# Kernel optimization log

Hardware: AMD Instinct MI355X
Metric: run time of the kernel (lower is better)

Reference implementation:

```python
import jax, jax.numpy as jnp
import numpy as np

G, N, H = 64, 512, 64          # graphs, nodes/graph, hidden
NT = G * N                     # total nodes
DEG = 32
ET = NT * DEG                  # total edges
KP = int(np.ceil(0.7 * N))     # TopKPooling keep per graph (359)
NP2 = G * KP                   # nodes after pooling
F_IN, NC, NA = 128, 2, 6
seg = jax.ops.segment_sum


def graph_norm(h, batch, num_g, w, b, ms, eps=1e-5):
    cnt = seg(jnp.ones((h.shape[0], 1), h.dtype), batch, num_segments=num_g)
    mean = seg(h, batch, num_segments=num_g) / cnt
    hc = h - ms * mean[batch]
    var = seg(hc * hc, batch, num_segments=num_g) / cnt
    return w * hc / jnp.sqrt(var[batch] + eps) + b


def sage(h, src, tgt, valid, Ws, Wn, b, n_nodes):
    # PyG SAGEConv (mean aggr): out_i = x_i@Ws + mean_{j->i} x_j @ Wn + b
    msg = h[src] * valid[:, None]
    agg = seg(msg, tgt, num_segments=n_nodes)
    deg = seg(valid, tgt, num_segments=n_nodes)
    return h @ Ws + (agg / jnp.maximum(deg, 1.0)[:, None]) @ Wn + b


def setup_inputs() -> dict:
    key = jax.random.key(0)
    ks = jax.random.split(key, 20)
    offs = (jnp.arange(G) * N)[:, None]
    src = (jax.random.randint(ks[0], (G, N * DEG), 0, N) + offs).reshape(-1)
    tgt = (jax.random.randint(ks[1], (G, N * DEG), 0, N) + offs).reshape(-1)
    edge_index = jnp.stack([src, tgt])  # within-graph edges

    def lin(k, fi, fo):
        return jax.random.normal(k, (fi, fo), jnp.float32) / np.sqrt(fi)

    return {
        "x": jax.random.normal(ks[2], (NT, F_IN), jnp.float32),
        "edge_index": edge_index,
        "edge_attr": jax.random.uniform(ks[3], (ET,), jnp.float32),
        "coords": jax.random.normal(ks[4], (NT, 3), jnp.float32),
        "anatomical_class": jax.random.randint(ks[5], (NT,), 0, NA),
        "Bk_table": jax.random.normal(ks[6], (NA, H * H), jnp.float32) * 0.05,
        "pos_W": lin(ks[7], 3, H), "pos_b": jnp.zeros((H,), jnp.float32),
        "W1_self": lin(ks[8], F_IN, H), "W1_neigh": lin(ks[9], F_IN, H),
        "b1": jnp.zeros((H,), jnp.float32),
        "gn1_w": jnp.ones((H,), jnp.float32), "gn1_b": jnp.zeros((H,), jnp.float32),
        "gn1_ms": jnp.ones((H,), jnp.float32),
        "pool_p": jax.random.normal(ks[10], (H,), jnp.float32),
        "W2_self": lin(ks[11], H, H), "W2_neigh": lin(ks[12], H, H),
        "b2": jnp.zeros((H,), jnp.float32),
        "gn2_w": jnp.ones((H,), jnp.float32), "gn2_b": jnp.zeros((H,), jnp.float32),
        "gn2_ms": jnp.ones((H,), jnp.float32),
        "lin1_W": lin(ks[13], 3 * H, H), "lin1_b": jnp.zeros((H,), jnp.float32),
        "lin2_W": lin(ks[14], H, NC), "lin2_b": jnp.zeros((NC,), jnp.float32),
    }


def reference(x, edge_index, edge_attr, coords, anatomical_class, Bk_table,
              pos_W, pos_b, W1_self, W1_neigh, b1, gn1_w, gn1_b, gn1_ms,
              pool_p, W2_self, W2_neigh, b2, gn2_w, gn2_b, gn2_ms,
              lin1_W, lin1_b, lin2_W, lin2_b):
    row, col = edge_index[0], edge_index[1]
    batch = jnp.repeat(jnp.arange(G), N)
    # ---- stage 1: anatomical propagation kernel ----
    e = coords @ pos_W + pos_b                                 # [NT, H]
    Ae = seg(edge_attr[:, None] * e[col], row, num_segments=NT)  # SpMM adj @ e
    Bk = Bk_table[anatomical_class].reshape(NT, H, H)
    delta = jnp.einsum('nd,nhd->nh', Ae, Bk)                   # bmm(Ae, Bk^T)
    ones_e = jnp.ones((ET,), x.dtype)
    h = sage(x, row, col, ones_e, W1_self, W1_neigh, b1, NT)
    h = jax.nn.elu(graph_norm(h, batch, G, gn1_w, gn1_b, gn1_ms))
    h = h + delta
    h = jnp.einsum('nij,nj->ni', Bk + delta[:, :, None], h)    # propagate_message
    # ---- TopK pooling (equal-sized graphs) ----
    score = (h @ pool_p) / jnp.linalg.norm(pool_p)
    vals, idx = jax.lax.top_k(score.reshape(G, N), KP)
    perm = (idx + (jnp.arange(G) * N)[:, None]).reshape(-1)    # [NP2]
    h = h[perm] * jnp.tanh(vals).reshape(-1)[:, None]
    batch2 = jnp.repeat(jnp.arange(G), KP)
    node_map = jnp.full((NT,), -1, jnp.int32).at[perm].set(jnp.arange(NP2, dtype=jnp.int32))
    s2, t2 = node_map[row], node_map[col]
    valid = ((s2 >= 0) & (t2 >= 0)).astype(h.dtype)            # masked edge filter
    s2 = jnp.where(s2 >= 0, s2, 0)
    t2 = jnp.where(t2 >= 0, t2, 0)
    # ---- stage 2 ----
    e2 = coords[perm] @ pos_W + pos_b
    Bk2 = Bk_table[anatomical_class[perm]].reshape(NP2, H, H)
    Ae2 = seg(valid[:, None] * e2[t2], s2, num_segments=NP2)   # edge_attr = ones
    delta2 = jnp.einsum('nd,nhd->nh', Ae2, Bk2)
    h = h + delta2
    h = jnp.einsum('nij,nj->ni', Bk2 + delta2[:, :, None], h)
    h = sage(h, s2, t2, valid, W2_self, W2_neigh, b2, NP2)
    h = jax.nn.elu(graph_norm(h, batch2, G, gn2_w, gn2_b, gn2_ms))
    # ---- readout ----
    cnt = seg(jnp.ones((NP2, 1), h.dtype), batch2, num_segments=G)
    hsum = seg(h, batch2, num_segments=G)
    g = jnp.concatenate([hsum / cnt,
                         jax.ops.segment_max(h, batch2, num_segments=G),
                         hsum], axis=1)
    g = jax.nn.relu(g @ lin1_W + lin1_b)
    return jax.nn.log_softmax(g @ lin2_W + lin2_b, axis=1)
```

## Files before the change

kernel.cpp:

```cpp
#include <hip/hip_runtime.h>
#include <math.h>

#define G_    64
#define N_    512
#define NT_   32768
#define ET_   1048576
#define EPG_  16384
#define KP_   359
#define NP2_  22976
#define FIN_  128

__global__ __launch_bounds__(256)
void k_histprep(const int* __restrict__ row, const int* __restrict__ col,
                int* __restrict__ histR8, int* __restrict__ histC8,
                const float* __restrict__ Bk, const float* __restrict__ posW,
                const float* __restrict__ posb,
                float* __restrict__ BkT, float* __restrict__ PT) {
    int b = blockIdx.x, t = threadIdx.x;
    if (b < 512) {
        __shared__ int hr[N_], hc[N_];
        int g = b >> 3, s = b & 7;
        for (int i = t; i < N_; i += 256) { hr[i] = 0; hc[i] = 0; }
        __syncthreads();
        int ebase = g * EPG_ + s * 2048;
        for (int i = t; i < 2048; i += 256) {
            atomicAdd(&hr[row[ebase + i] & (N_ - 1)], 1);
            atomicAdd(&hc[col[ebase + i] & (N_ - 1)], 1);
        }
        __syncthreads();
        int sbase = b * N_;
        for (int i = t; i < N_; i += 256) {
            histR8[sbase + i] = hr[i];
            histC8[sbase + i] = hc[i];
        }
    } else if (b < 608) {
        int idx = (b - 512) * 256 + t;
        int c = idx >> 12, r = idx & 4095;
        int h = r >> 6, d = r & 63;
        BkT[c*4096 + d*64 + h] = Bk[c*4096 + h*64 + d];
    } else {
        int c = b - 608;
        int i = t >> 6, h = t & 63;
        const float* B = Bk + c*4096 + h*64;
        float acc = 0.f;
        for (int d = 0; d < 64; d++) {
            float vd = (i < 3) ? posW[i*64 + d] : posb[d];
            acc += B[d] * vd;
        }
        PT[c*256 + i*64 + h] = acc;
    }
}

__global__ __launch_bounds__(256)
void k_gemm_dual(const float* __restrict__ in, int K,
                 const float* __restrict__ Wa, const float* __restrict__ Wb,
                 const float* __restrict__ bias,
                 float* __restrict__ outA, float* __restrict__ outB) {
    __shared__ float inT[32 * FIN_];
    int row0 = blockIdx.x * 32;
    int t = threadIdx.x;
    for (int idx = t; idx < 32 * K; idx += 256) inT[idx] = in[row0 * K + idx];
    __syncthreads();
    int c = t & 63, rb = t >> 6;
    const float* ip = inT + (rb * 8) * K;
    float aA[8] = {0,0,0,0,0,0,0,0};
    float aB[8] = {0,0,0,0,0,0,0,0};
    for (int k = 0; k < K; k += 4) {
        float wa0 = Wa[(k+0)*64 + c], wa1 = Wa[(k+1)*64 + c];
        float wa2 = Wa[(k+2)*64 + c], wa3 = Wa[(k+3)*64 + c];
        float wb0 = Wb[(k+0)*64 + c], wb1 = Wb[(k+1)*64 + c];
        float wb2 = Wb[(k+2)*64 + c], wb3 = Wb[(k+3)*64 + c];
        #pragma unroll
        for (int r = 0; r < 8; r++) {
            float4 xv = *(const float4*)&ip[r*K + k];
            aA[r] += xv.x*wa0; aB[r] += xv.x*wb0;
            aA[r] += xv.y*wa1; aB[r] += xv.y*wb1;
            aA[r] += xv.z*wa2; aB[r] += xv.z*wb2;
            aA[r] += xv.w*wa3; aB[r] += xv.w*wb3;
        }
    }
    float bv = bias[c];
    #pragma unroll
    for (int r = 0; r < 8; r++) {
        int node = row0 + rb*8 + r;
        outA[node*64 + c] = aA[r];
        outB[node*64 + c] = aB[r] + bv;
    }
}

__global__ __launch_bounds__(1024)
void k_scatfuse(const int* __restrict__ row, const int* __restrict__ col,
                const float* __restrict__ ea,
                const int* __restrict__ histR8, const int* __restrict__ histC8,
                const float* __restrict__ coords, const float* __restrict__ y,
                const float* __restrict__ hself,
                int2* __restrict__ rowcsr, int* __restrict__ colcsr,
                int* __restrict__ rowptr, int* __restrict__ colptr,
                float* __restrict__ deg, int* __restrict__ nmap,
                float4* __restrict__ nsum, float* __restrict__ agg,
                float* __restrict__ statsP) {
    __shared__ int hr[N_], hc[N_];
    __shared__ int rst[128], rcn[128], cst[128], ccn[128];
    __shared__ float red[2048];
    int g = blockIdx.x >> 2, q = blockIdx.x & 3;
    int t = threadIdx.x;
    int lo = q * 128;
    int nbase = g * N_, ebase = g * EPG_;
    for (int i = t; i < N_; i += 1024) {
        int sr = 0, sc = 0;
        #pragma unroll
        for (int s = 0; s < 8; s++) {
            sr += histR8[(g*8 + s)*N_ + i];
            sc += histC8[(g*8 + s)*N_ + i];
        }
        hr[i] = sr; hc[i] = sc;
    }
    __syncthreads();
    int wave = t >> 6, lane = t & 63;
    if (wave < 2) {
        int* h = wave ? hc : hr;
        int base8 = lane * 8;
        int loc[8];
        int tot = 0;
        #pragma unroll
        for (int i = 0; i < 8; i++) { int v = h[base8 + i]; loc[i] = tot; tot += v; }
        int pref = tot;
        for (int off = 1; off < 64; off <<= 1) {
            int u = __shfl_up(pref, off);
            if (lane >= off) pref += u;
        }
        pref -= tot;
        #pragma unroll
        for (int i = 0; i < 8; i++) h[base8 + i] = pref + loc[i];
    }
    __syncthreads();
    if (t < 128) {
        int i = lo + t;
        int rs = hr[i];
        int re = (i < N_ - 1) ? hr[i + 1] : EPG_;
        int cs = hc[i];
        int ce = (i < N_ - 1) ? hc[i + 1] : EPG_;
        rst[t] = ebase + rs; rcn[t] = re - rs;
        cst[t] = ebase + cs; ccn[t] = ce - cs;
        rowptr[nbase + i] = ebase + rs;
        colptr[nbase + i] = ebase + cs;
        deg[nbase + i] = (float)(ce - cs);
        nmap[nbase + i] = -1;
    }
    if (blockIdx.x == 0 && t == 0) { rowptr[NT_] = ET_; colptr[NT_] = ET_; }
    __syncthreads();
    for (int i = t; i < EPG_; i += 1024) {
        int rg = row[ebase + i];
        int cg = col[ebase + i];
        int rl = (rg & (N_ - 1)) - lo;
        if ((unsigned)rl < 128u) {
            int pr = atomicAdd(&hr[lo + rl], 1);
            rowcsr[ebase + pr] = make_int2(cg, __float_as_int(ea[ebase + i]));
        }
        int cl = (cg & (N_ - 1)) - lo;
        if ((unsigned)cl < 128u) {
            int pc = atomicAdd(&hc[lo + cl], 1);
            colcsr[ebase + pc] = rg;
        }
    }
    __threadfence_block();
    __syncthreads();
    float s1 = 0.f, s2 = 0.f;
    #pragma unroll
    for (int r = 0; r < 8; r++) {
        int li   = wave * 8 + r;
        int node = nbase + lo + li;
        int rs = rst[li], rc = rcn[li];
        float sx = 0.f, sy = 0.f, sz = 0.f, sw = 0.f;
        for (int k = lane; k < rc; k += 64) {
            int2 ent = rowcsr[rs + k];
            int c = ent.x;
            float w = __int_as_float(ent.y);
            sx += w * coords[c*3+0];
            sy += w * coords[c*3+1];
            sz += w * coords[c*3+2];
            sw += w;
        }
        #pragma unroll
        for (int off = 32; off; off >>= 1) {
            sx += __shfl_xor(sx, off); sy += __shfl_xor(sy, off);
            sz += __shfl_xor(sz, off); sw += __shfl_xor(sw, off);
        }
        if (lane == 0) nsum[node] = make_float4(sx, sy, sz, sw);
        int cs = cst[li], cc = ccn[li];
        float acc = 0.f;
        #pragma unroll 8
        for (int k = 0; k < cc; k++) {
            int rr = colcsr[cs + k];
            acc += y[rr*64 + lane];
        }
        agg[node*64 + lane] = acc;
        float v = hself[node*64 + lane] + acc / fmaxf((float)cc, 1.f);
        s1 += v; s2 += v * v;
    }
    red[wave*64 + lane]        = s1;
    red[1024 + wave*64 + lane] = s2;
    __syncthreads();
    if (t < 64) {
        float a1 = 0.f, a2 = 0.f;
        #pragma unroll
        for (int wv = 0; wv < 16; wv++) {
            a1 += red[wv*64 + t];
            a2 += red[1024 + wv*64 + t];
        }
        statsP[blockIdx.x*128 + t]      = a1;
        statsP[blockIdx.x*128 + 64 + t] = a2;
    }
}

__global__ __launch_bounds__(256)
void k_gnstat(const float* __restrict__ hs, const float* __restrict__ agg,
              const float* __restrict__ deg, float* __restrict__ partial,
              int NPG, int CH, int npc) {
    __shared__ float r1[256], r2[256];
    int b = blockIdx.x;
    int g = b / CH, chunk = b % CH;
    int t = threadIdx.x, c = t & 63, grp = t >> 6;
    int n0 = chunk * npc;
    int nend = min(n0 + npc, NPG);
    float s1 = 0.f, s2 = 0.f;
    for (int n = n0 + grp; n < nend; n += 4) {
        int node = g * NPG + n;
        float v = hs[node*64 + c] + agg[node*64 + c] / fmaxf(deg[node], 1.f);
        s1 += v; s2 += v * v;
    }
    r1[t] = s1; r2[t] = s2;
    __syncthreads();
    if (grp == 0) {
        partial[b*128 + c]      = r1[c] + r1[64+c] + r1[128+c] + r1[192+c];
        partial[b*128 + 64 + c] = r2[c] + r2[64+c] + r2[128+c] + r2[192+c];
    }
}

__global__ __launch_bounds__(256)
void k_gnprop(const float* __restrict__ hself, const float* __restrict__ agg,
              const float* __restrict__ deg, const float* __restrict__ partial,
              const float* __restrict__ ms,
              const float* __restrict__ w, const float* __restrict__ b,
              const float4* __restrict__ nsum, const int* __restrict__ cls,
              const float* __restrict__ PT, const float* __restrict__ BkT,
              float* __restrict__ out) {
    __shared__ float hT[256];
    int t = threadIdx.x;
    int node = blockIdx.x * 4 + (t >> 6);
    int lane = t & 63;
    int g = (blockIdx.x * 4) >> 9;
    float s1 = 0.f, s2 = 0.f;
    #pragma unroll
    for (int i = 0; i < 4; i++) {
        s1 += partial[(g*4 + i)*128 + lane];
        s2 += partial[(g*4 + i)*128 + 64 + lane];
    }
    float m  = s1 / (float)N_, q = s2 / (float)N_, msv = ms[lane];
    float var = q - msv * m * m * (2.f - msv);
    float mval = msv * m;
    float istd = rsqrtf(var + 1e-5f);
    float4 s4 = nsum[node];
    int c = cls[node];
    const float* P = PT + c * 256;
    float d = s4.x*P[lane] + s4.y*P[64+lane] + s4.z*P[128+lane] + s4.w*P[192+lane];
    float v = hself[node*64 + lane] + agg[node*64 + lane] / fmaxf(deg[node], 1.f);
    v = w[lane] * (v - mval) * istd + b[lane];
    v = v > 0.f ? v : expm1f(v);
    v += d;
    hT[t] = v;
    __syncthreads();
    float ssum = v;
    #pragma unroll
    for (int off = 32; off; off >>= 1) ssum += __shfl_xor(ssum, off);
    const float* B  = BkT + c * 4096;
    const float* hv = hT + (t & ~63);
    float acc = 0.f;
    #pragma unroll 8
    for (int j = 0; j < 64; j++) acc += B[j*64 + lane] * hv[j];
    out[node*64 + lane] = acc + d * ssum;
}

__global__ __launch_bounds__(512)
void k_topk(const float* __restrict__ hp, const float* __restrict__ p,
            const int* __restrict__ cls, const int* __restrict__ ccsr,
            const int* __restrict__ row, const int* __restrict__ col,
            int* __restrict__ perm, float* __restrict__ tanhv,
            int* __restrict__ node_map, int* __restrict__ class2,
            int* __restrict__ ccsr2, float* __restrict__ deg2) {
    __shared__ float key[N_];
    __shared__ int   idxS[N_];
    __shared__ int   lmap[N_];
    __shared__ int   ideg[KP_];
    __shared__ float pS[64];
    __shared__ float nrm;
    int g = blockIdx.x, t = threadIdx.x;
    lmap[t] = -1;
    if (t < 64) pS[t] = p[t];
    for (int i = t; i < KP_; i += 512) ideg[i] = 0;
    __syncthreads();
    if (t == 0) {
        float s = 0.f;
        for (int i = 0; i < 64; i++) s += pS[i] * pS[i];
        nrm = sqrtf(s);
    }
    __syncthreads();
    {
        float acc = 0.f;
        const float* hv = hp + (size_t)(g*N_ + t) * 64;
        for (int cdx = 0; cdx < 64; cdx++) acc += hv[cdx] * pS[cdx];
        key[t]  = acc / nrm;
        idxS[t] = t;
    }
    __syncthreads();
    for (int k = 2; k <= N_; k <<= 1) {
        for (int j = k >> 1; j > 0; j >>= 1) {
            int i = t, ixj = i ^ j;
            if (ixj > i) {
                float ki = key[i], kj = key[ixj];
                int   ii = idxS[i], ij = idxS[ixj];
                bool before = (ki > kj) || (ki == kj && ii < ij);
                bool dir = ((i & k) == 0);
                if (dir ? !before : before) {
                    key[i] = kj; key[ixj] = ki;
                    idxS[i] = ij; idxS[ixj] = ii;
                }
            }
            __syncthreads();
        }
    }
    if (t < KP_) {
        int orig  = idxS[t];
        int gnode = g * N_ + orig;
        int pj    = g * KP_ + t;
        perm[pj]     = gnode;
        tanhv[pj]    = tanhf(key[t]);
        node_map[gnode] = pj;
        class2[pj]   = cls[gnode];
        lmap[orig]   = pj;
    }
    __syncthreads();
    int ebase = g * EPG_;
    for (int k = t; k < EPG_; k += 512) {
        int mm = lmap[ccsr[ebase + k] & (N_ - 1)];
        ccsr2[ebase + k] = (mm >= 0) ? mm : NP2_;
    }
    for (int k = t; k < EPG_; k += 512) {
        int mr = lmap[row[ebase + k] & (N_ - 1)];
        int mc = lmap[col[ebase + k] & (N_ - 1)];
        if (mr >= 0 && mc >= 0) atomicAdd(&ideg[mc - g * KP_], 1);
    }
    __syncthreads();
    for (int i = t; i < KP_; i += 512) deg2[g * KP_ + i] = (float)ideg[i];
}

__global__ __launch_bounds__(256)
void k_s2prop(const int* __restrict__ rowptr, const int2* __restrict__ rcsr,
              const int* __restrict__ perm, const int* __restrict__ nmap,
              const float* __restrict__ coords,
              const float* __restrict__ hp, const float* __restrict__ tanhv,
              const int* __restrict__ cls2,
              const float* __restrict__ PT, const float* __restrict__ BkT,
              float* __restrict__ out, float* __restrict__ y2zero) {
    __shared__ float hT[256];
    int t = threadIdx.x;
    int j = blockIdx.x * 4 + (t >> 6);
    int lane = t & 63;
    if (blockIdx.x == 0 && t < 64) y2zero[t] = 0.f;
    int orig = perm[j];
    int rs = rowptr[orig], re = rowptr[orig + 1];
    float sx = 0.f, sy = 0.f, sz = 0.f, sw = 0.f;
    for (int k = rs + lane; k < re; k += 64) {
        int c = rcsr[k].x;
        if (nmap[c] >= 0) {
            sx += coords[c*3+0]; sy += coords[c*3+1]; sz += coords[c*3+2];
            sw += 1.f;
        }
    }
    #pragma unroll
    for (int off = 32; off; off >>= 1) {
        sx += __shfl_xor(sx, off); sy += __shfl_xor(sy, off);
        sz += __shfl_xor(sz, off); sw += __shfl_xor(sw, off);
    }
    int c = cls2[j];
    const float* P = PT + c * 256;
    float d = sx*P[lane] + sy*P[64+lane] + sz*P[128+lane] + sw*P[192+lane];
    float v = hp[orig*64 + lane] * tanhv[j] + d;
    hT[t] = v;
    __syncthreads();
    float ssum = v;
    #pragma unroll
    for (int off = 32; off; off >>= 1) ssum += __shfl_xor(ssum, off);
    const float* B  = BkT + c * 4096;
    const float* hv = hT + (t & ~63);
    float acc = 0.f;
    #pragma unroll 8
    for (int jj = 0; jj < 64; jj++) acc += B[jj*64 + lane] * hv[jj];
    out[j*64 + lane] = acc + d * ssum;
}

__global__ __launch_bounds__(256)
void k_gagg2(const int* __restrict__ colptr, const int* __restrict__ ccsr2,
             const int* __restrict__ perm, const float* __restrict__ y2,
             float* __restrict__ agg2) {
    int j = blockIdx.x * 4 + (threadIdx.x >> 6);
    int lane = threadIdx.x & 63;
    int orig = perm[j];
    int start = colptr[orig], end = colptr[orig + 1];
    float acc = 0.f;
    #pragma unroll 8
    for (int k = start; k < end; k++) {
        int r = ccsr2[k];
        acc += y2[r*64 + lane];
    }
    agg2[j*64 + lane] = acc;
}

__global__ __launch_bounds__(256)
void k_gnrd(const float* __restrict__ hs, const float* __restrict__ agg,
            const float* __restrict__ deg2, const float* __restrict__ statsP,
            const float* __restrict__ ms,
            const float* __restrict__ w, const float* __restrict__ b,
            float* __restrict__ readP) {
    __shared__ float r1[256], r2[256];
    int blk = blockIdx.x;
    int g = blk / 6, chunk = blk % 6;
    int t = threadIdx.x, c = t & 63, grp = t >> 6;
    float s1 = 0.f, s2 = 0.f;
    #pragma unroll
    for (int i = 0; i < 6; i++) {
        s1 += statsP[(g*6 + i)*128 + c];
        s2 += statsP[(g*6 + i)*128 + 64 + c];
    }
    float mean = s1 / (float)KP_, q = s2 / (float)KP_, msv = ms[c];
    float var = q - msv * mean * mean * (2.f - msv);
    float mv = msv * mean;
    float is = rsqrtf(var + 1e-5f);
    float wv = w[c], bv = b[c];
    int n0 = chunk * 60, nend = min(n0 + 60, KP_);
    float s = 0.f, m = -1e30f;
    for (int n = n0 + grp; n < nend; n += 4) {
        int node = g * KP_ + n;
        float v = hs[node*64 + c] + agg[node*64 + c] / fmaxf(deg2[node], 1.f);
        v = wv * (v - mv) * is + bv;
        v = v > 0.f ? v : expm1f(v);
        s += v; m = fmaxf(m, v);
    }
    r1[t] = s; r2[t] = m;
    __syncthreads();
    if (grp == 0) {
        readP[blk*128 + c]      = r1[c] + r1[64+c] + r1[128+c] + r1[192+c];
        readP[blk*128 + 64 + c] = fmaxf(fmaxf(r2[c], r2[64+c]), fmaxf(r2[128+c], r2[192+c]));
    }
}

__global__ void k_rfin(const float* __restrict__ part, int CH,
                       const float* __restrict__ l1W, const float* __restrict__ l1b,
                       const float* __restrict__ l2W, const float* __restrict__ l2b,
                       float* __restrict__ out) {
    __shared__ float gv[192], rS[64];
    int g = blockIdx.x, t = threadIdx.x;
    float s = 0.f, m = -1e30f;
    for (int i = 0; i < CH; i++) {
        s += part[(g*CH + i)*128 + t];
        m = fmaxf(m, part[(g*CH + i)*128 + 64 + t]);
    }
    gv[t] = s / (float)KP_;
    gv[64 + t] = m;
    gv[128 + t] = s;
    __syncthreads();
    float acc = l1b[t];
    for (int k = 0; k < 192; k++) acc += gv[k] * l1W[k*64 + t];
    rS[t] = fmaxf(acc, 0.f);
    __syncthreads();
    if (t == 0) {
        float l0 = l2b[0], l1v = l2b[1];
        for (int hh = 0; hh < 64; hh++) { l0 += rS[hh]*l2W[hh*2+0]; l1v += rS[hh]*l2W[hh*2+1]; }
        float mx  = fmaxf(l0, l1v);
        float lse = mx + logf(expf(l0 - mx) + expf(l1v - mx));
        out[g*2 + 0] = l0  - lse;
        out[g*2 + 1] = l1v - lse;
    }
}

extern "C" void kernel_launch(void* const* d_in, const int* in_sizes, int n_in,
                              void* d_out, int out_size, void* d_ws, size_t ws_size,
                              hipStream_t stream) {
    const float* x      = (const float*)d_in[0];
    const int*   eidx   = (const int*)  d_in[1];
    const float* eattr  = (const float*)d_in[2];
    const float* coords = (const float*)d_in[3];
    const int*   acls   = (const int*)  d_in[4];
    const float* BkTab  = (const float*)d_in[5];
    const float* posW   = (const float*)d_in[6];
    const float* posb   = (const float*)d_in[7];
    const float* W1s    = (const float*)d_in[8];
    const float* W1n    = (const float*)d_in[9];
    const float* b1     = (const float*)d_in[10];
    const float* gn1w   = (const float*)d_in[11];
    const float* gn1b   = (const float*)d_in[12];
    const float* gn1ms  = (const float*)d_in[13];
    const float* poolp  = (const float*)d_in[14];
    const float* W2s    = (const float*)d_in[15];
    const float* W2n    = (const float*)d_in[16];
    const float* b2     = (const float*)d_in[17];
    const float* gn2w   = (const float*)d_in[18];
    const float* gn2b   = (const float*)d_in[19];
    const float* gn2ms  = (const float*)d_in[20];
    const float* l1W    = (const float*)d_in[21];
    const float* l1b    = (const float*)d_in[22];
    const float* l2W    = (const float*)d_in[23];
    const float* l2b    = (const float*)d_in[24];

    const int* row  = eidx;
    const int* colp = eidx + ET_;

    float* W = (float*)d_ws;
    const size_t NTH = (size_t)NT_ * 64;
    float* b0    = W;
    float* b1buf = W + 1*NTH;
    float* b2buf = W + 2*NTH;
    float* b3buf = W + 3*NTH;
    float* p = W + 4*NTH;
    int2*  rowcsr = (int2*)p;        p += 2*(size_t)ET_;
    int*   colcsr = (int*)p;         p += ET_;
    int*   ccsr2  = (int*)p;         p += ET_;
    int*   rowptr = (int*)p;         p += NT_ + 8;
    int*   colptr = (int*)p;         p += NT_ + 8;
    int*   histR8 = (int*)p;         p += NT_ * 8;
    int*   histC8 = (int*)p;         p += NT_ * 8;
    float* deg    = p;               p += NT_;
    float* deg2   = p;               p += NP2_;
    float* tanhv  = p;               p += NP2_;
    int*   perm   = (int*)p;         p += NP2_;
    int*   nmap   = (int*)p;         p += NT_;
    int*   cls2   = (int*)p;         p += NP2_;
    float* BkT    = p;               p += 6 * 4096;
    float* PT     = p;               p += 6 * 256;
    float* statsP = p;               p += (size_t)G_ * 8 * 128;
    float* readP  = p;               p += (size_t)G_ * 6 * 128;
    float4* nsum  = (float4*)b3buf;

    k_histprep <<<614,     256,  0, stream>>>(row, colp, histR8, histC8,
                                              BkTab, posW, posb, BkT, PT);
    k_gemm_dual<<<NT_/32,  256, 0, stream>>>(x, FIN_, W1n, W1s, b1,
                                             b0 , b1buf );
    k_scatfuse <<<G_*4,    1024, 0, stream>>>(row, colp, eattr, histR8, histC8,
                                              coords, b0 , b1buf ,
                                              rowcsr, colcsr, rowptr, colptr,
                                              deg, nmap, nsum, b2buf ,
                                              statsP);
    k_gnprop   <<<NT_/4,   256, 0, stream>>>(b1buf , b2buf , deg,
                                             statsP, gn1ms, gn1w, gn1b,
                                             nsum, acls, PT, BkT,
                                             b1buf );
    k_topk     <<<G_,      512, 0, stream>>>(b1buf , poolp, acls, colcsr,
                                             row, colp, perm, tanhv, nmap,
                                             cls2, ccsr2, deg2);

    k_s2prop   <<<NP2_/4,  256, 0, stream>>>(rowptr, rowcsr, perm, nmap, coords,
                                             b1buf , tanhv, cls2, PT, BkT,
                                             b2buf ,
                                             b0 + (size_t)NP2_ * 64 );
    k_gemm_dual<<<NP2_/32, 256, 0, stream>>>(b2buf , 64, W2n, W2s, b2,
                                             b0 , b3buf );
    k_gagg2    <<<NP2_/4,  256, 0, stream>>>(colptr, ccsr2, perm, b0 ,
                                             b1buf );
    k_gnstat   <<<G_*6,    256, 0, stream>>>(b3buf , b1buf , deg2,
                                             statsP, KP_, 6, 60);
    k_gnrd     <<<G_*6,    256, 0, stream>>>(b3buf , b1buf , deg2,
                                             statsP, gn2ms, gn2w, gn2b, readP);
    k_rfin     <<<G_,      64,  0, stream>>>(readP, 6, l1W, l1b, l2W, l2b,
                                             (float*)d_out);
}
```

Baseline: 341.7 us.

## Restructure stage-1 pipeline: merge gemm with histogram prep, split scatter from aggregation

The first GEMM is merged into the histogram/Bk-prep launch, so one kernel covers both. The heavy per-graph scatter kernel, which ran only 256 blocks of 1024 threads, is split into a CSR-building scan kernel and a separate per-node edge aggregation kernel with far more blocks, followed by a standalone GraphNorm stats pass. The pre-normalisation value (self + mean aggregate) is materialised once in a buffer, so the stats and normalise kernels no longer recompute it from agg/deg. This adds one extra launch and an extra 64-wide buffer write/read in exchange for better parallelism in the aggregation stage.

```diff
diff --git a/kernel.cpp b/kernel.cpp
--- a/kernel.cpp
+++ b/kernel.cpp
@@ -10,55 +10,13 @@
 #define NP2_  22976
 #define FIN_  128
 
-__global__ __launch_bounds__(256)
-void k_histprep(const int* __restrict__ row, const int* __restrict__ col,
-                int* __restrict__ histR8, int* __restrict__ histC8,
-                const float* __restrict__ Bk, const float* __restrict__ posW,
-                const float* __restrict__ posb,
-                float* __restrict__ BkT, float* __restrict__ PT) {
-    int b = blockIdx.x, t = threadIdx.x;
-    if (b < 512) {
-        __shared__ int hr[N_], hc[N_];
-        int g = b >> 3, s = b & 7;
-        for (int i = t; i < N_; i += 256) { hr[i] = 0; hc[i] = 0; }
-        __syncthreads();
-        int ebase = g * EPG_ + s * 2048;
-        for (int i = t; i < 2048; i += 256) {
-            atomicAdd(&hr[row[ebase + i] & (N_ - 1)], 1);
-            atomicAdd(&hc[col[ebase + i] & (N_ - 1)], 1);
-        }
-        __syncthreads();
-        int sbase = b * N_;
-        for (int i = t; i < N_; i += 256) {
-            histR8[sbase + i] = hr[i];
-            histC8[sbase + i] = hc[i];
-        }
-    } else if (b < 608) {
-        int idx = (b - 512) * 256 + t;
-        int c = idx >> 12, r = idx & 4095;
-        int h = r >> 6, d = r & 63;
-        BkT[c*4096 + d*64 + h] = Bk[c*4096 + h*64 + d];
-    } else {
-        int c = b - 608;
-        int i = t >> 6, h = t & 63;
-        const float* B = Bk + c*4096 + h*64;
-        float acc = 0.f;
-        for (int d = 0; d < 64; d++) {
-            float vd = (i < 3) ? posW[i*64 + d] : posb[d];
-            acc += B[d] * vd;
-        }
-        PT[c*256 + i*64 + h] = acc;
-    }
-}
-
-__global__ __launch_bounds__(256)
-void k_gemm_dual(const float* __restrict__ in, int K,
-                 const float* __restrict__ Wa, const float* __restrict__ Wb,
-                 const float* __restrict__ bias,
-                 float* __restrict__ outA, float* __restrict__ outB) {
-    __shared__ float inT[32 * FIN_];
-    int row0 = blockIdx.x * 32;
-    int t = threadIdx.x;
+__device__ __forceinline__
+void gemm_unit(int unit, const float* __restrict__ in, int K,
+               const float* __restrict__ Wa, const float* __restrict__ Wb,
+               const float* __restrict__ bias,
+               float* __restrict__ outA, float* __restrict__ outB,
+               float* inT, int t) {
+    int row0 = unit * 32;
     for (int idx = t; idx < 32 * K; idx += 256) inT[idx] = in[row0 * K + idx];
     __syncthreads();
     int c = t & 63, rb = t >> 6;
@@ -88,20 +46,63 @@
     }
 }
 
+__global__ __launch_bounds__(256)
+void k_pregemm(const float* __restrict__ x,
+               const float* __restrict__ W1n, const float* __restrict__ W1s,
+               const float* __restrict__ b1,
+               float* __restrict__ y, float* __restrict__ hself,
+               const int* __restrict__ row, const int* __restrict__ col,
+               int* __restrict__ histR8, int* __restrict__ histC8,
+               const float* __restrict__ Bk, const float* __restrict__ posW,
+               const float* __restrict__ posb,
+               float* __restrict__ BkT, float* __restrict__ PT) {
+    __shared__ float smem[32 * FIN_];
+    int b = blockIdx.x, t = threadIdx.x;
+    if (b < NT_/32) {
+        gemm_unit(b, x, FIN_, W1n, W1s, b1, y, hself, smem, t);
+    } else if (b < NT_/32 + 512) {
+        int bb = b - NT_/32;
+        int* hr = (int*)smem; int* hc = hr + N_;
+        int g = bb >> 3, s = bb & 7;
+        for (int i = t; i < N_; i += 256) { hr[i] = 0; hc[i] = 0; }
+        __syncthreads();
+        int ebase = g * EPG_ + s * 2048;
+        for (int i = t; i < 2048; i += 256) {
+            atomicAdd(&hr[row[ebase + i] & (N_ - 1)], 1);
+            atomicAdd(&hc[col[ebase + i] & (N_ - 1)], 1);
+        }
+        __syncthreads();
+        int sbase = bb * N_;
+        for (int i = t; i < N_; i += 256) {
+            histR8[sbase + i] = hr[i];
+            histC8[sbase + i] = hc[i];
+        }
+    } else if (b < NT_/32 + 608) {
+        int idx = (b - NT_/32 - 512) * 256 + t;
+        int c = idx >> 12, r = idx & 4095;
+        int h = r >> 6, d = r & 63;
+        BkT[c*4096 + d*64 + h] = Bk[c*4096 + h*64 + d];
+    } else {
+        int c = b - (NT_/32 + 608);
+        int i = t >> 6, h = t & 63;
+        const float* B = Bk + c*4096 + h*64;
+        float acc = 0.f;
+        for (int d = 0; d < 64; d++) {
+            float vd = (i < 3) ? posW[i*64 + d] : posb[d];
+            acc += B[d] * vd;
+        }
+        PT[c*256 + i*64 + h] = acc;
+    }
+}
+
 __global__ __launch_bounds__(1024)
-void k_scatfuse(const int* __restrict__ row, const int* __restrict__ col,
+void k_scatscan(const int* __restrict__ row, const int* __restrict__ col,
                 const float* __restrict__ ea,
                 const int* __restrict__ histR8, const int* __restrict__ histC8,
-                const float* __restrict__ coords, const float* __restrict__ y,
-                const float* __restrict__ hself,
                 int2* __restrict__ rowcsr, int* __restrict__ colcsr,
                 int* __restrict__ rowptr, int* __restrict__ colptr,
-                float* __restrict__ deg, int* __restrict__ nmap,
-                float4* __restrict__ nsum, float* __restrict__ agg,
-                float* __restrict__ statsP) {
+                int* __restrict__ nmap) {
     __shared__ int hr[N_], hc[N_];
-    __shared__ int rst[128], rcn[128], cst[128], ccn[128];
-    __shared__ float red[2048];
     int g = blockIdx.x >> 2, q = blockIdx.x & 3;
     int t = threadIdx.x;
     int lo = q * 128;
@@ -136,15 +137,8 @@
     __syncthreads();
     if (t < 128) {
         int i = lo + t;
-        int rs = hr[i];
-        int re = (i < N_ - 1) ? hr[i + 1] : EPG_;
-        int cs = hc[i];
-        int ce = (i < N_ - 1) ? hc[i + 1] : EPG_;
-        rst[t] = ebase + rs; rcn[t] = re - rs;
-        cst[t] = ebase + cs; ccn[t] = ce - cs;
-        rowptr[nbase + i] = ebase + rs;
-        colptr[nbase + i] = ebase + cs;
-        deg[nbase + i] = (float)(ce - cs);
+        rowptr[nbase + i] = ebase + hr[i];
+        colptr[nbase + i] = ebase + hc[i];
         nmap[nbase + i] = -1;
     }
     if (blockIdx.x == 0 && t == 0) { rowptr[NT_] = ET_; colptr[NT_] = ET_; }
@@ -163,59 +157,45 @@
             colcsr[ebase + pc] = rg;
         }
     }
-    __threadfence_block();
-    __syncthreads();
-    float s1 = 0.f, s2 = 0.f;
-    #pragma unroll
-    for (int r = 0; r < 8; r++) {
-        int li   = wave * 8 + r;
-        int node = nbase + lo + li;
-        int rs = rst[li], rc = rcn[li];
-        float sx = 0.f, sy = 0.f, sz = 0.f, sw = 0.f;
-        for (int k = lane; k < rc; k += 64) {
-            int2 ent = rowcsr[rs + k];
-            int c = ent.x;
-            float w = __int_as_float(ent.y);
-            sx += w * coords[c*3+0];
-            sy += w * coords[c*3+1];
-            sz += w * coords[c*3+2];
-            sw += w;
-        }
-        #pragma unroll
-        for (int off = 32; off; off >>= 1) {
-            sx += __shfl_xor(sx, off); sy += __shfl_xor(sy, off);
-            sz += __shfl_xor(sz, off); sw += __shfl_xor(sw, off);
-        }
-        if (lane == 0) nsum[node] = make_float4(sx, sy, sz, sw);
-        int cs = cst[li], cc = ccn[li];
-        float acc = 0.f;
-        #pragma unroll 8
-        for (int k = 0; k < cc; k++) {
-            int rr = colcsr[cs + k];
-            acc += y[rr*64 + lane];
-        }
-        agg[node*64 + lane] = acc;
-        float v = hself[node*64 + lane] + acc / fmaxf((float)cc, 1.f);
-        s1 += v; s2 += v * v;
-    }
-    red[wave*64 + lane]        = s1;
-    red[1024 + wave*64 + lane] = s2;
-    __syncthreads();
-    if (t < 64) {
-        float a1 = 0.f, a2 = 0.f;
-        #pragma unroll
-        for (int wv = 0; wv < 16; wv++) {
-            a1 += red[wv*64 + t];
-            a2 += red[1024 + wv*64 + t];
-        }
-        statsP[blockIdx.x*128 + t]      = a1;
-        statsP[blockIdx.x*128 + 64 + t] = a2;
-    }
-}
-
-__global__ __launch_bounds__(256)
-void k_gnstat(const float* __restrict__ hs, const float* __restrict__ agg,
-              const float* __restrict__ deg, float* __restrict__ partial,
+}
+
+__global__ __launch_bounds__(256)
+void k_edge1f(const int* __restrict__ rowptr, const int2* __restrict__ rcsr,
+              const int* __restrict__ colptr, const int* __restrict__ ccsr,
+              const float* __restrict__ coords, const float* __restrict__ y,
+              const float* __restrict__ hself,
+              float4* __restrict__ nsum, float* __restrict__ vbuf) {
+    int node = blockIdx.x * 4 + (threadIdx.x >> 6);
+    int lane = threadIdx.x & 63;
+    int rs = rowptr[node], re = rowptr[node + 1];
+    float sx = 0.f, sy = 0.f, sz = 0.f, sw = 0.f;
+    for (int k = rs + lane; k < re; k += 64) {
+        int2 ent = rcsr[k];
+        int c = ent.x;
+        float w = __int_as_float(ent.y);
+        sx += w * coords[c*3+0];
+        sy += w * coords[c*3+1];
+        sz += w * coords[c*3+2];
+        sw += w;
+    }
+    #pragma unroll
+    for (int off = 32; off; off >>= 1) {
+        sx += __shfl_xor(sx, off); sy += __shfl_xor(sy, off);
+        sz += __shfl_xor(sz, off); sw += __shfl_xor(sw, off);
+    }
+    if (lane == 0) nsum[node] = make_float4(sx, sy, sz, sw);
+    int cs = colptr[node], ce = colptr[node + 1];
+    float acc = 0.f;
+    #pragma unroll 8
+    for (int k = cs; k < ce; k++) {
+        int r = ccsr[k];
+        acc += y[r*64 + lane];
+    }
+    vbuf[node*64 + lane] = hself[node*64 + lane] + acc / fmaxf((float)(ce - cs), 1.f);
+}
+
+__global__ __launch_bounds__(256)
+void k_gnstat(const float* __restrict__ v, float* __restrict__ partial,
               int NPG, int CH, int npc) {
     __shared__ float r1[256], r2[256];
     int b = blockIdx.x;
@@ -225,9 +205,8 @@
     int nend = min(n0 + npc, NPG);
     float s1 = 0.f, s2 = 0.f;
     for (int n = n0 + grp; n < nend; n += 4) {
-        int node = g * NPG + n;
-        float v = hs[node*64 + c] + agg[node*64 + c] / fmaxf(deg[node], 1.f);
-        s1 += v; s2 += v * v;
+        float vv = v[(g * NPG + n)*64 + c];
+        s1 += vv; s2 += vv * vv;
     }
     r1[t] = s1; r2[t] = s2;
     __syncthreads();
@@ -238,8 +217,7 @@
 }
 
 __global__ __launch_bounds__(256)
-void k_gnprop(const float* __restrict__ hself, const float* __restrict__ agg,
-              const float* __restrict__ deg, const float* __restrict__ partial,
+void k_gnprop(const float* __restrict__ vbuf, const float* __restrict__ partial,
               const float* __restrict__ ms,
               const float* __restrict__ w, const float* __restrict__ b,
               const float4* __restrict__ nsum, const int* __restrict__ cls,
@@ -252,9 +230,9 @@
     int g = (blockIdx.x * 4) >> 9;
     float s1 = 0.f, s2 = 0.f;
     #pragma unroll
-    for (int i = 0; i < 4; i++) {
-        s1 += partial[(g*4 + i)*128 + lane];
-        s2 += partial[(g*4 + i)*128 + 64 + lane];
+    for (int i = 0; i < 8; i++) {
+        s1 += partial[(g*8 + i)*128 + lane];
+        s2 += partial[(g*8 + i)*128 + 64 + lane];
     }
     float m  = s1 / (float)N_, q = s2 / (float)N_, msv = ms[lane];
     float var = q - msv * m * m * (2.f - msv);
@@ -264,7 +242,7 @@
     int c = cls[node];
     const float* P = PT + c * 256;
     float d = s4.x*P[lane] + s4.y*P[64+lane] + s4.z*P[128+lane] + s4.w*P[192+lane];
-    float v = hself[node*64 + lane] + agg[node*64 + lane] / fmaxf(deg[node], 1.f);
+    float v = vbuf[node*64 + lane];
     v = w[lane] * (v - mval) * istd + b[lane];
     v = v > 0.f ? v : expm1f(v);
     v += d;
@@ -400,9 +378,19 @@
 }
 
 __global__ __launch_bounds__(256)
-void k_gagg2(const int* __restrict__ colptr, const int* __restrict__ ccsr2,
-             const int* __restrict__ perm, const float* __restrict__ y2,
-             float* __restrict__ agg2) {
+void k_gemm2(const float* __restrict__ in,
+             const float* __restrict__ Wa, const float* __restrict__ Wb,
+             const float* __restrict__ bias,
+             float* __restrict__ outA, float* __restrict__ outB) {
+    __shared__ float inT[32 * 64];
+    gemm_unit(blockIdx.x, in, 64, Wa, Wb, bias, outA, outB, inT, threadIdx.x);
+}
+
+__global__ __launch_bounds__(256)
+void k_gagg2v(const int* __restrict__ colptr, const int* __restrict__ ccsr2,
+              const int* __restrict__ perm, const float* __restrict__ y2,
+              const float* __restrict__ hs2, const float* __restrict__ deg2,
+              float* __restrict__ v2buf) {
     int j = blockIdx.x * 4 + (threadIdx.x >> 6);
     int lane = threadIdx.x & 63;
     int orig = perm[j];
@@ -413,12 +401,11 @@
         int r = ccsr2[k];
         acc += y2[r*64 + lane];
     }
-    agg2[j*64 + lane] = acc;
-}
-
-__global__ __launch_bounds__(256)
-void k_gnrd(const float* __restrict__ hs, const float* __restrict__ agg,
-            const float* __restrict__ deg2, const float* __restrict__ statsP,
+    v2buf[j*64 + lane] = hs2[j*64 + lane] + acc / fmaxf(deg2[j], 1.f);
+}
+
+__global__ __launch_bounds__(256)
+void k_gnrd(const float* __restrict__ v2, const float* __restrict__ statsP,
             const float* __restrict__ ms,
             const float* __restrict__ w, const float* __restrict__ b,
             float* __restrict__ readP) {
@@ -440,8 +427,7 @@
     int n0 = chunk * 60, nend = min(n0 + 60, KP_);
     float s = 0.f, m = -1e30f;
     for (int n = n0 + grp; n < nend; n += 4) {
-        int node = g * KP_ + n;
-        float v = hs[node*64 + c] + agg[node*64 + c] / fmaxf(deg2[node], 1.f);
+        float v = v2[(g * KP_ + n)*64 + c];
         v = wv * (v - mv) * is + bv;
         v = v > 0.f ? v : expm1f(v);
         s += v; m = fmaxf(m, v);
@@ -529,7 +515,6 @@
     int*   colptr = (int*)p;         p += NT_ + 8;
     int*   histR8 = (int*)p;         p += NT_ * 8;
     int*   histC8 = (int*)p;         p += NT_ * 8;
-    float* deg    = p;               p += NT_;
     float* deg2   = p;               p += NP2_;
     float* tanhv  = p;               p += NP2_;
     int*   perm   = (int*)p;         p += NP2_;
@@ -541,18 +526,18 @@
     float* readP  = p;               p += (size_t)G_ * 6 * 128;
     float4* nsum  = (float4*)b3buf;
 
-    k_histprep <<<614,     256,  0, stream>>>(row, colp, histR8, histC8,
-                                              BkTab, posW, posb, BkT, PT);
-    k_gemm_dual<<<NT_/32,  256, 0, stream>>>(x, FIN_, W1n, W1s, b1,
-                                             b0 , b1buf );
-    k_scatfuse <<<G_*4,    1024, 0, stream>>>(row, colp, eattr, histR8, histC8,
-                                              coords, b0 , b1buf ,
-                                              rowcsr, colcsr, rowptr, colptr,
-                                              deg, nmap, nsum, b2buf ,
-                                              statsP);
-    k_gnprop   <<<NT_/4,   256, 0, stream>>>(b1buf , b2buf , deg,
-                                             statsP, gn1ms, gn1w, gn1b,
-                                             nsum, acls, PT, BkT,
+    k_pregemm  <<<NT_/32 + 614, 256, 0, stream>>>(x, W1n, W1s, b1,
+                                                  b0 , b1buf ,
+                                                  row, colp, histR8, histC8,
+                                                  BkTab, posW, posb, BkT, PT);
+    k_scatscan <<<G_*4,    1024, 0, stream>>>(row, colp, eattr, histR8, histC8,
+                                              rowcsr, colcsr, rowptr, colptr, nmap);
+    k_edge1f   <<<NT_/4,   256, 0, stream>>>(rowptr, rowcsr, colptr, colcsr,
+                                             coords, b0 , b1buf ,
+                                             nsum, b2buf );
+    k_gnstat   <<<G_*8,    256, 0, stream>>>(b2buf , statsP, N_, 8, 64);
+    k_gnprop   <<<NT_/4,   256, 0, stream>>>(b2buf , statsP, gn1ms,
+                                             gn1w, gn1b, nsum, acls, PT, BkT,
                                              b1buf );
     k_topk     <<<G_,      512, 0, stream>>>(b1buf , poolp, acls, colcsr,
                                              row, colp, perm, tanhv, nmap,
@@ -562,14 +547,14 @@
                                              b1buf , tanhv, cls2, PT, BkT,
                                              b2buf ,
                                              b0 + (size_t)NP2_ * 64 );
-    k_gemm_dual<<<NP2_/32, 256, 0, stream>>>(b2buf , 64, W2n, W2s, b2,
+    k_gemm2    <<<NP2_/32, 256, 0, stream>>>(b2buf , W2n, W2s, b2,
                                              b0 , b3buf );
-    k_gagg2    <<<NP2_/4,  256, 0, stream>>>(colptr, ccsr2, perm, b0 ,
+    k_gagg2v   <<<NP2_/4,  256, 0, stream>>>(colptr, ccsr2, perm, b0 ,
+                                             b3buf , deg2,
                                              b1buf );
-    k_gnstat   <<<G_*6,    256, 0, stream>>>(b3buf , b1buf , deg2,
-                                             statsP, KP_, 6, 60);
-    k_gnrd     <<<G_*6,    256, 0, stream>>>(b3buf , b1buf , deg2,
-                                             statsP, gn2ms, gn2w, gn2b, readP);
+    k_gnstat   <<<G_*6,    256, 0, stream>>>(b1buf , statsP, KP_, 6, 60);
+    k_gnrd     <<<G_*6,    256, 0, stream>>>(b1buf , statsP, gn2ms,
+                                             gn2w, gn2b, readP);
     k_rfin     <<<G_,      64,  0, stream>>>(readP, 6, l1W, l1b, l2W, l2b,
                                              (float*)d_out);
 }
```

Measured after the change: 333.7 us (median of 2 runs). 2.4% less time.
